# Performance work log

Measured on AMD Instinct MI355X. Metric: run time of the kernel, lower is better.

## Reference

```python
import jax, jax.numpy as jnp
import numpy as np

T, B, IN, H1, HB = 512, 256, 64, 128, 32  # seq, batch, input, LSTM width, bottleneck


def _lstm(x, w_ih, w_hh, b_ih, b_hh):
    """Single-layer unidirectional LSTM, time-major x: [T,B,in] -> [T,B,H].
    PyTorch gate order: i, f, g, o. Zero initial state."""
    H = w_hh.shape[1]
    # hoist input projection out of the scan: [T,B,4H]
    xg = jnp.einsum('tbi,gi->tbg', x, w_ih) + b_ih + b_hh

    def step(carry, xt):
        h, c = carry
        g = xt + h @ w_hh.T
        i, f, gg, o = jnp.split(g, 4, axis=-1)
        c = jax.nn.sigmoid(f) * c + jax.nn.sigmoid(i) * jnp.tanh(gg)
        h = jax.nn.sigmoid(o) * jnp.tanh(c)
        return (h, c), h

    h0 = jnp.zeros((x.shape[1], H), x.dtype)
    (_, _), hs = jax.lax.scan(step, (h0, h0), xg)
    return hs


def setup_inputs() -> dict:
    key = jax.random.key(0)
    ks = jax.random.split(key, 17)
    s = 0.05

    def p(k, shape):
        return jax.random.normal(k, shape, dtype=jnp.float32) * s

    return {
        'X': jax.random.normal(ks[0], (T, B, IN), dtype=jnp.float32),
        # en1: IN -> H1
        'w1_ih': p(ks[1], (4 * H1, IN)), 'w1_hh': p(ks[2], (4 * H1, H1)),
        'b1_ih': p(ks[3], (4 * H1,)), 'b1_hh': p(ks[4], (4 * H1,)),
        # en2: H1 -> HB
        'w2_ih': p(ks[5], (4 * HB, H1)), 'w2_hh': p(ks[6], (4 * HB, HB)),
        'b2_ih': p(ks[7], (4 * HB,)), 'b2_hh': p(ks[8], (4 * HB,)),
        # de1: HB -> H1
        'w3_ih': p(ks[9], (4 * H1, HB)), 'w3_hh': p(ks[10], (4 * H1, H1)),
        'b3_ih': p(ks[11], (4 * H1,)), 'b3_hh': p(ks[12], (4 * H1,)),
        # de2: H1 -> IN
        'w4_ih': p(ks[13], (4 * IN, H1)), 'w4_hh': p(ks[14], (4 * IN, IN)),
        'b4_ih': p(ks[15], (4 * IN,)), 'b4_hh': p(ks[16], (4 * IN,)),
    }


def reference(X, w1_ih, w1_hh, b1_ih, b1_hh, w2_ih, w2_hh, b2_ih, b2_hh,
              w3_ih, w3_hh, b3_ih, b3_hh, w4_ih, w4_hh, b4_ih, b4_hh):
    h = _lstm(X, w1_ih, w1_hh, b1_ih, b1_hh)      # [T,B,128]
    h = _lstm(h, w2_ih, w2_hh, b2_ih, b2_hh)      # [T,B,32]
    h = jnp.tanh(h)                               # bottleneck tanh
    h = _lstm(h, w3_ih, w3_hh, b3_ih, b3_hh)      # [T,B,128]
    out = _lstm(h, w4_ih, w4_hh, b4_ih, b4_hh)    # [T,B,64]
    return out
```

## Files before the change

kernel.cpp:

```cpp
#include <hip/hip_runtime.h>

#define T_STEPS 512
#define BATCH   256

typedef _Float16 f16;
typedef unsigned long long u64;
typedef __attribute__((ext_vector_type(8))) _Float16 f16x8;
typedef __attribute__((ext_vector_type(4))) _Float16 f16x4;
typedef __attribute__((ext_vector_type(4))) float    f32x4;

#define L2E 1.44269504088896340736f

__device__ __forceinline__ float rcp_f(float x)  { return __builtin_amdgcn_rcpf(x); }
__device__ __forceinline__ float exp2_f(float x) { return __builtin_amdgcn_exp2f(x); }

__device__ __forceinline__ float tanh_n(float x) {
    return fmaf(-2.0f, rcp_f(1.0f + exp2_f(2.0f * L2E * x)), 1.0f);
}
__device__ __forceinline__ u64 tanh4_f16(u64 v) {
    f16x4 h = __builtin_bit_cast(f16x4, v);
    f16x4 r;
#pragma unroll
    for (int i = 0; i < 4; ++i) r[i] = (f16)tanh_n((float)h[i]);
    return __builtin_bit_cast(u64, r);
}

__device__ __forceinline__ void barrier_lgkm() {
    asm volatile("s_waitcnt lgkmcnt(0)\n\ts_barrier" ::: "memory");
}
__device__ __forceinline__ void barrier_drain() {
    asm volatile("s_waitcnt vmcnt(0) lgkmcnt(0)\n\ts_barrier" ::: "memory");
}

__device__ __forceinline__ int  flag_load(const int* p) {
    return __hip_atomic_load(p, __ATOMIC_RELAXED, __HIP_MEMORY_SCOPE_AGENT);
}
__device__ __forceinline__ void flag_store(int* p, int v) {
    __hip_atomic_store(p, v, __ATOMIC_RELAXED, __HIP_MEMORY_SCOPE_AGENT);
}
__device__ __forceinline__ u64  panel_load(const u64* p) {
    return __hip_atomic_load(p, __ATOMIC_RELAXED, __HIP_MEMORY_SCOPE_AGENT);
}
__device__ __forceinline__ void panel_store(u64* p, u64 v) {
    __hip_atomic_store(p, v, __ATOMIC_RELAXED, __HIP_MEMORY_SCOPE_AGENT);
}

template <int IN_DIM, int H, bool IN_F32, bool OUT_PANEL, bool OUT_TANH>
__device__ __forceinline__ void lstm_layer_dev(
    char* sm,
    const void* __restrict__ xv,
    const int* in_flag,
    int* out_flag,
    const float* __restrict__ w_ih, const float* __restrict__ w_hh,
    const float* __restrict__ b_ih, const float* __restrict__ b_hh,
    void* __restrict__ outv,
    int group, int ltid)
{
    constexpr int KTX = IN_DIM / 32, KTH = H / 32, KT = KTX + KTH;
    constexpr int XP = IN_DIM + 8, HP = H + 8, NT = 4 * H;

    f16 (*xs)[16][XP] = (f16(*)[16][XP])sm;
    f16 (*hs)[16][HP] = (f16(*)[16][HP])(sm + 2 * 16 * XP * 2);

    const int wave = ltid >> 6, lane = ltid & 63;
    const int col = lane & 15, q = lane >> 4;
    const int bblk = group * 16;
    const int u = wave * 16 + col;

    f16x8 bw[4][KT];
#pragma unroll
    for (int g = 0; g < 4; ++g) {
        const float sc = (g == 2) ? 2.0f * L2E : L2E;
        const int row = g * H + u;
#pragma unroll
        for (int kt = 0; kt < KTX; ++kt) {
            const float* p = w_ih + (size_t)row * IN_DIM + kt * 32 + q * 8;
            f16x8 v;
#pragma unroll
            for (int j = 0; j < 8; ++j) v[j] = (f16)(p[j] * sc);
            bw[g][kt] = v;
        }
#pragma unroll
        for (int kt = 0; kt < KTH; ++kt) {
            const float* p = w_hh + (size_t)row * H + kt * 32 + q * 8;
            f16x8 v;
#pragma unroll
            for (int j = 0; j < 8; ++j) v[j] = (f16)(p[j] * sc);
            bw[g][KTX + kt] = v;
        }
    }
    float bias[4];
#pragma unroll
    for (int g = 0; g < 4; ++g)
        bias[g] = (b_ih[g * H + u] + b_hh[g * H + u]) * ((g == 2) ? 2.0f * L2E : L2E);
    float cst[4] = {0.f, 0.f, 0.f, 0.f};

    constexpr int ELD = IN_F32 ? 4 : 8;
    constexpr int EPR = IN_DIM / ELD;
    constexpr int NCH = 16 * EPR;
    constexpr int CPT = (NCH + NT - 1) / NT;
    constexpr long XADVB = (long)BATCH * IN_DIM * (IN_F32 ? 4 : 2);
    bool sv[CPT]; const char* sgp[CPT]; f16* slp[CPT];
    constexpr int LDSD = 16 * XP;
#pragma unroll
    for (int k = 0; k < CPT; ++k) {
        const int cc = ltid + k * NT;
        sv[k] = (cc < NCH);
        const int r_ = (cc < NCH ? cc : 0) / EPR;
        const int o_ = (cc < NCH ? cc : 0) % EPR;
        sgp[k] = (const char*)xv + ((size_t)(bblk + r_) * IN_DIM + o_ * ELD) * (IN_F32 ? 4 : 2);
        slp[k] = &xs[0][r_][o_ * ELD];
    }

    constexpr int OEPR = H / 4;
    u64* opg = nullptr;
    f16* olds = nullptr;
    float* outp_f32 = nullptr;
    if constexpr (OUT_PANEL) {
        const int orow = ltid / OEPR, ooff = ltid % OEPR;
        opg  = (u64*)((f16*)outv + (size_t)(bblk + orow) * H) + ooff;
        olds = &hs[0][orow][ooff * 4];
    } else {
        outp_f32 = (float*)outv + ((size_t)bblk + 4 * q) * H + u;
    }
    constexpr int HLDSD = 16 * HP;

    for (int i = ltid; i < 16 * HP; i += NT) hs[0][i / HP][i % HP] = (f16)0.f;
    int seen = 0;
    if constexpr (!IN_F32) {
        do { seen = flag_load(in_flag); } while (seen < 1);
    }
#pragma unroll
    for (int k = 0; k < CPT; ++k) {
        if (sv[k]) {
            if constexpr (IN_F32) {
                const f32x4 v = *reinterpret_cast<const f32x4*>(sgp[k]);
                f16x4 h4;
                h4[0] = (f16)v[0]; h4[1] = (f16)v[1]; h4[2] = (f16)v[2]; h4[3] = (f16)v[3];
                *reinterpret_cast<f16x4*>(slp[k]) = h4;
            } else {
                u64 a = panel_load((const u64*)sgp[k]);
                u64 b = panel_load((const u64*)sgp[k] + 1);
                u64 pk[2] = {a, b};
                *reinterpret_cast<f16x8*>(slp[k]) = *reinterpret_cast<const f16x8*>(pk);
            }
            sgp[k] += XADVB;
        }
    }
    barrier_drain();

    float hold[4] = {0.f, 0.f, 0.f, 0.f};

    auto step = [&](int t, int pbv, bool dodrain, bool dopub) {
        if constexpr (OUT_PANEL) {
            if (dopub && t >= 4 && ltid == 0) flag_store(out_flag, t - 1);
        }

        f32x4 xr32[CPT]; u64 xr16[CPT][2];
        const bool pf = (t + 1 < T_STEPS);
        if (pf) {
            if constexpr (!IN_F32) {
                if (seen < t + 2) {
                    do { seen = flag_load(in_flag); } while (seen < t + 2);
                }
            }
#pragma unroll
            for (int k = 0; k < CPT; ++k) {
                if (sv[k]) {
                    if constexpr (IN_F32) {
                        xr32[k] = *reinterpret_cast<const f32x4*>(sgp[k]);
                    } else {
                        xr16[k][0] = panel_load((const u64*)sgp[k]);
                        xr16[k][1] = panel_load((const u64*)sgp[k] + 1);
                    }
                    sgp[k] += XADVB;
                }
            }
        }

        if (t >= 1) {
            if constexpr (OUT_PANEL) {
                u64 v = *reinterpret_cast<const u64*>(olds + pbv * HLDSD);
                if constexpr (OUT_TANH) v = tanh4_f16(v);
                panel_store(opg, v);
                opg += (size_t)BATCH * H / 4;
            } else {
#pragma unroll
                for (int r = 0; r < 4; ++r) outp_f32[r * H] = hold[r];
                outp_f32 += (size_t)BATCH * H;
            }
        }

        f16x8 a[KT];
#pragma unroll
        for (int kt = 0; kt < KTX; ++kt)
            a[kt] = *reinterpret_cast<const f16x8*>(&xs[pbv][col][kt * 32 + q * 8]);
#pragma unroll
        for (int kt = 0; kt < KTH; ++kt)
            a[KTX + kt] = *reinterpret_cast<const f16x8*>(&hs[pbv][col][kt * 32 + q * 8]);

        f32x4 accX[4], accH[4];
#pragma unroll
        for (int g = 0; g < 4; ++g) {
            accX[g] = (f32x4){bias[g], bias[g], bias[g], bias[g]};
            accH[g] = (f32x4){0.f, 0.f, 0.f, 0.f};
        }
#pragma unroll
        for (int kt = 0; kt < KTX; ++kt)
#pragma unroll
            for (int g = 0; g < 4; ++g)
                accX[g] = __builtin_amdgcn_mfma_f32_16x16x32_f16(a[kt], bw[g][kt], accX[g], 0, 0, 0);
#pragma unroll
        for (int kt = 0; kt < KTH; ++kt)
#pragma unroll
            for (int g = 0; g < 4; ++g)
                accH[g] = __builtin_amdgcn_mfma_f32_16x16x32_f16(a[KTX + kt], bw[g][KTX + kt], accH[g], 0, 0, 0);

#pragma unroll
        for (int r = 0; r < 4; ++r) {
            const float yi = accX[0][r] + accH[0][r];
            const float yf = accX[1][r] + accH[1][r];
            const float yg = accX[2][r] + accH[2][r];
            const float yo = accX[3][r] + accH[3][r];
            const float Ei = exp2_f(-yi);
            const float G  = exp2_f(yg);
            const float Ef = exp2_f(-yf);
            const float sf = rcp_f(1.0f + Ef);
            const float itg = (2.0f * L2E) * (G - 1.0f) *
                              rcp_f((1.0f + Ei) * (G + 1.0f));
            cst[r] = fmaf(sf, cst[r], itg);
            const float C  = exp2_f(cst[r]);
            const float Eo = exp2_f(-yo);
            const float h  = (C - 1.0f) * rcp_f((1.0f + Eo) * (C + 1.0f));
            hs[pbv ^ 1][4 * q + r][u] = (f16)h;
            if constexpr (!OUT_PANEL) hold[r] = h;
        }

        if (pf) {
#pragma unroll
            for (int k = 0; k < CPT; ++k) {
                if (sv[k]) {
                    f16* dst = slp[k] + (pbv ^ 1) * LDSD;
                    if constexpr (IN_F32) {
                        f16x4 h4;
                        h4[0] = (f16)xr32[k][0]; h4[1] = (f16)xr32[k][1];
                        h4[2] = (f16)xr32[k][2]; h4[3] = (f16)xr32[k][3];
                        *reinterpret_cast<f16x4*>(dst) = h4;
                    } else {
                        *reinterpret_cast<f16x8*>(dst) =
                            *reinterpret_cast<const f16x8*>(xr16[k]);
                    }
                }
            }
        }

        if constexpr (!IN_F32) {
            if (dopub && seen < t + 9) seen = flag_load(in_flag);
        }

        if (dodrain) barrier_drain(); else barrier_lgkm();
    };

    for (int tb = 0; tb < T_STEPS; tb += 4) {
        step(tb + 0, 0, false, true);
        step(tb + 1, 1, false, false);
        step(tb + 2, 0, false, false);
        step(tb + 3, 1, true,  false);
    }

    if constexpr (OUT_PANEL) {
        u64 v = *reinterpret_cast<const u64*>(olds);
        if constexpr (OUT_TANH) v = tanh4_f16(v);
        panel_store(opg, v);
    } else {
#pragma unroll
        for (int r = 0; r < 4; ++r) outp_f32[r * H] = hold[r];
    }
    barrier_drain();
    if constexpr (OUT_PANEL) {
        if (ltid == 0) flag_store(out_flag, T_STEPS + 4);
    }
}

__global__ __launch_bounds__(512, 1)
void lstm_fused(const float* __restrict__ X,
                const float* __restrict__ w1_ih, const float* __restrict__ w1_hh,
                const float* __restrict__ b1_ih, const float* __restrict__ b1_hh,
                const float* __restrict__ w2_ih, const float* __restrict__ w2_hh,
                const float* __restrict__ b2_ih, const float* __restrict__ b2_hh,
                const float* __restrict__ w3_ih, const float* __restrict__ w3_hh,
                const float* __restrict__ b3_ih, const float* __restrict__ b3_hh,
                const float* __restrict__ w4_ih, const float* __restrict__ w4_hh,
                const float* __restrict__ b4_ih, const float* __restrict__ b4_hh,
                f16* __restrict__ h1, f16* __restrict__ h2, f16* __restrict__ h3,
                int* __restrict__ flags, float* __restrict__ out)
{
    __shared__ __attribute__((aligned(16))) char smem[45056];
    const int b = blockIdx.x, tid = threadIdx.x;

    if (b < 16) {
        lstm_layer_dev<64, 128, true, true, false>(
            smem, X, nullptr, flags + 0 * 16 + b,
            w1_ih, w1_hh, b1_ih, b1_hh, h1, b, tid);
    } else if (b < 20) {
        const int gl = tid >> 7;
        const int g  = (b - 16) * 4 + gl;
        lstm_layer_dev<128, 32, false, true, true>(
            smem + gl * 11264, h1, flags + 0 * 16 + g, flags + 1 * 16 + g,
            w2_ih, w2_hh, b2_ih, b2_hh, h2, g, tid & 127);
    } else if (b < 36) {
        const int g = b - 20;
        lstm_layer_dev<32, 128, false, true, false>(
            smem, h2, flags + 1 * 16 + g, flags + 2 * 16 + g,
            w3_ih, w3_hh, b3_ih, b3_hh, h3, g, tid);
    } else {
        const int gl = tid >> 8;
        const int g  = (b - 36) * 2 + gl;
        lstm_layer_dev<128, 64, false, false, false>(
            smem + gl * 13312, h3, flags + 2 * 16 + g, nullptr,
            w4_ih, w4_hh, b4_ih, b4_hh, out, g, tid & 255);
    }
}

extern "C" void kernel_launch(void* const* d_in, const int* in_sizes, int n_in,
                              void* d_out, int out_size, void* d_ws, size_t ws_size,
                              hipStream_t stream) {
    const float* X     = (const float*)d_in[0];
    const float* w1_ih = (const float*)d_in[1];
    const float* w1_hh = (const float*)d_in[2];
    const float* b1_ih = (const float*)d_in[3];
    const float* b1_hh = (const float*)d_in[4];
    const float* w2_ih = (const float*)d_in[5];
    const float* w2_hh = (const float*)d_in[6];
    const float* b2_ih = (const float*)d_in[7];
    const float* b2_hh = (const float*)d_in[8];
    const float* w3_ih = (const float*)d_in[9];
    const float* w3_hh = (const float*)d_in[10];
    const float* b3_ih = (const float*)d_in[11];
    const float* b3_hh = (const float*)d_in[12];
    const float* w4_ih = (const float*)d_in[13];
    const float* w4_hh = (const float*)d_in[14];
    const float* b4_ih = (const float*)d_in[15];
    const float* b4_hh = (const float*)d_in[16];

    float* out = (float*)d_out;

    int* flags = (int*)d_ws;
    f16* h1 = (f16*)((char*)d_ws + 256);
    f16* h2 = h1 + (size_t)T_STEPS * BATCH * 128;
    f16* h3 = h2 + (size_t)T_STEPS * BATCH * 32;

    lstm_fused<<<44, 512, 0, stream>>>(X,
        w1_ih, w1_hh, b1_ih, b1_hh, w2_ih, w2_hh, b2_ih, b2_hh,
        w3_ih, w3_hh, b3_ih, b3_hh, w4_ih, w4_hh, b4_ih, b4_hh,
        h1, h2, h3, flags, out);
}
```

Baseline: 667.0 us.

## Prefetch LSTM inputs two steps ahead and merge gate accumulators

The per-step global load of next-timestep inputs becomes a two-deep register pipeline: loads for step t+2 are issued during step t, using alternating odd/even register sets, and the drain barrier waits only until the newest loads remain outstanding. The separate input and hidden MFMA accumulators are merged into one chain seeded with the bias. This aims to hide global and inter-layer panel load latency behind the recurrent compute and to remove the final adds. In exchange it uses more registers, and the single accumulator chain lengthens the MFMA dependency chain.

```diff
diff --git a/kernel.cpp b/kernel.cpp
--- a/kernel.cpp
+++ b/kernel.cpp
@@ -30,6 +30,17 @@
 }
 __device__ __forceinline__ void barrier_drain() {
     asm volatile("s_waitcnt vmcnt(0) lgkmcnt(0)\n\ts_barrier" ::: "memory");
+}
+template <int K>
+__device__ __forceinline__ void barrier_drain_k() {
+    if constexpr (K == 1)
+        asm volatile("s_waitcnt vmcnt(1) lgkmcnt(0)\n\ts_barrier" ::: "memory");
+    else if constexpr (K == 2)
+        asm volatile("s_waitcnt vmcnt(2) lgkmcnt(0)\n\ts_barrier" ::: "memory");
+    else if constexpr (K == 4)
+        asm volatile("s_waitcnt vmcnt(4) lgkmcnt(0)\n\ts_barrier" ::: "memory");
+    else
+        asm volatile("s_waitcnt vmcnt(0) lgkmcnt(0)\n\ts_barrier" ::: "memory");
 }
 
 __device__ __forceinline__ int  flag_load(const int* p) {
@@ -99,6 +110,7 @@
     constexpr int EPR = IN_DIM / ELD;
     constexpr int NCH = 16 * EPR;
     constexpr int CPT = (NCH + NT - 1) / NT;
+    constexpr int NLOAD = IN_F32 ? CPT : 2 * CPT;
     constexpr long XADVB = (long)BATCH * IN_DIM * (IN_F32 ? 4 : 2);
     bool sv[CPT]; const char* sgp[CPT]; f16* slp[CPT];
     constexpr int LDSD = 16 * XP;
@@ -147,35 +159,32 @@
             sgp[k] += XADVB;
         }
     }
-    barrier_drain();
+    f32x4 xr32O[CPT], xr32E[CPT];
+    u64 xr16O[CPT][2], xr16E[CPT][2];
+    if constexpr (!IN_F32) {
+        if (seen < 2) { do { seen = flag_load(in_flag); } while (seen < 2); }
+    }
+#pragma unroll
+    for (int k = 0; k < CPT; ++k) {
+        if (sv[k]) {
+            if constexpr (IN_F32) {
+                xr32O[k] = *reinterpret_cast<const f32x4*>(sgp[k]);
+            } else {
+                xr16O[k][0] = panel_load((const u64*)sgp[k]);
+                xr16O[k][1] = panel_load((const u64*)sgp[k] + 1);
+            }
+            sgp[k] += XADVB;
+        }
+    }
+    barrier_lgkm();
 
     float hold[4] = {0.f, 0.f, 0.f, 0.f};
 
-    auto step = [&](int t, int pbv, bool dodrain, bool dopub) {
+    auto step = [&](int t, int pbv, bool dodrain, bool dopub,
+                    f32x4 (&c32)[CPT], f32x4 (&i32)[CPT],
+                    u64 (&c16)[CPT][2], u64 (&i16)[CPT][2]) {
         if constexpr (OUT_PANEL) {
             if (dopub && t >= 4 && ltid == 0) flag_store(out_flag, t - 1);
-        }
-
-        f32x4 xr32[CPT]; u64 xr16[CPT][2];
-        const bool pf = (t + 1 < T_STEPS);
-        if (pf) {
-            if constexpr (!IN_F32) {
-                if (seen < t + 2) {
-                    do { seen = flag_load(in_flag); } while (seen < t + 2);
-                }
-            }
-#pragma unroll
-            for (int k = 0; k < CPT; ++k) {
-                if (sv[k]) {
-                    if constexpr (IN_F32) {
-                        xr32[k] = *reinterpret_cast<const f32x4*>(sgp[k]);
-                    } else {
-                        xr16[k][0] = panel_load((const u64*)sgp[k]);
-                        xr16[k][1] = panel_load((const u64*)sgp[k] + 1);
-                    }
-                    sgp[k] += XADVB;
-                }
-            }
         }
 
         if (t >= 1) {
@@ -191,6 +200,27 @@
             }
         }
 
+        const bool iss = (t + 2 < T_STEPS);
+        if (iss) {
+            if constexpr (!IN_F32) {
+                if (seen < t + 3) {
+                    do { seen = flag_load(in_flag); } while (seen < t + 3);
+                }
+            }
+#pragma unroll
+            for (int k = 0; k < CPT; ++k) {
+                if (sv[k]) {
+                    if constexpr (IN_F32) {
+                        i32[k] = *reinterpret_cast<const f32x4*>(sgp[k]);
+                    } else {
+                        i16[k][0] = panel_load((const u64*)sgp[k]);
+                        i16[k][1] = panel_load((const u64*)sgp[k] + 1);
+                    }
+                    sgp[k] += XADVB;
+                }
+            }
+        }
+
         f16x8 a[KT];
 #pragma unroll
         for (int kt = 0; kt < KTX; ++kt)
@@ -199,29 +229,22 @@
         for (int kt = 0; kt < KTH; ++kt)
             a[KTX + kt] = *reinterpret_cast<const f16x8*>(&hs[pbv][col][kt * 32 + q * 8]);
 
-        f32x4 accX[4], accH[4];
-#pragma unroll
-        for (int g = 0; g < 4; ++g) {
-            accX[g] = (f32x4){bias[g], bias[g], bias[g], bias[g]};
-            accH[g] = (f32x4){0.f, 0.f, 0.f, 0.f};
-        }
-#pragma unroll
-        for (int kt = 0; kt < KTX; ++kt)
+        f32x4 acc[4];
+#pragma unroll
+        for (int g = 0; g < 4; ++g)
+            acc[g] = (f32x4){bias[g], bias[g], bias[g], bias[g]};
+#pragma unroll
+        for (int kt = 0; kt < KT; ++kt)
 #pragma unroll
             for (int g = 0; g < 4; ++g)
-                accX[g] = __builtin_amdgcn_mfma_f32_16x16x32_f16(a[kt], bw[g][kt], accX[g], 0, 0, 0);
-#pragma unroll
-        for (int kt = 0; kt < KTH; ++kt)
-#pragma unroll
-            for (int g = 0; g < 4; ++g)
-                accH[g] = __builtin_amdgcn_mfma_f32_16x16x32_f16(a[KTX + kt], bw[g][KTX + kt], accH[g], 0, 0, 0);
+                acc[g] = __builtin_amdgcn_mfma_f32_16x16x32_f16(a[kt], bw[g][kt], acc[g], 0, 0, 0);
 
 #pragma unroll
         for (int r = 0; r < 4; ++r) {
-            const float yi = accX[0][r] + accH[0][r];
-            const float yf = accX[1][r] + accH[1][r];
-            const float yg = accX[2][r] + accH[2][r];
-            const float yo = accX[3][r] + accH[3][r];
+            const float yi = acc[0][r];
+            const float yf = acc[1][r];
+            const float yg = acc[2][r];
+            const float yo = acc[3][r];
             const float Ei = exp2_f(-yi);
             const float G  = exp2_f(yg);
             const float Ef = exp2_f(-yf);
@@ -236,6 +259,7 @@
             if constexpr (!OUT_PANEL) hold[r] = h;
         }
 
+        const bool pf = (t + 1 < T_STEPS);
         if (pf) {
 #pragma unroll
             for (int k = 0; k < CPT; ++k) {
@@ -243,12 +267,12 @@
                     f16* dst = slp[k] + (pbv ^ 1) * LDSD;
                     if constexpr (IN_F32) {
                         f16x4 h4;
-                        h4[0] = (f16)xr32[k][0]; h4[1] = (f16)xr32[k][1];
-                        h4[2] = (f16)xr32[k][2]; h4[3] = (f16)xr32[k][3];
+                        h4[0] = (f16)c32[k][0]; h4[1] = (f16)c32[k][1];
+                        h4[2] = (f16)c32[k][2]; h4[3] = (f16)c32[k][3];
                         *reinterpret_cast<f16x4*>(dst) = h4;
                     } else {
                         *reinterpret_cast<f16x8*>(dst) =
-                            *reinterpret_cast<const f16x8*>(xr16[k]);
+                            *reinterpret_cast<const f16x8*>(c16[k]);
                     }
                 }
             }
@@ -258,14 +282,14 @@
             if (dopub && seen < t + 9) seen = flag_load(in_flag);
         }
 
-        if (dodrain) barrier_drain(); else barrier_lgkm();
+        if (dodrain) barrier_drain_k<NLOAD>(); else barrier_lgkm();
     };
 
     for (int tb = 0; tb < T_STEPS; tb += 4) {
-        step(tb + 0, 0, false, true);
-        step(tb + 1, 1, false, false);
-        step(tb + 2, 0, false, false);
-        step(tb + 3, 1, true,  false);
+        step(tb + 0, 0, false, true,  xr32O, xr32E, xr16O, xr16E);
+        step(tb + 1, 1, false, false, xr32E, xr32O, xr16E, xr16O);
+        step(tb + 2, 0, false, false, xr32O, xr32E, xr16O, xr16E);
+        step(tb + 3, 1, true,  false, xr32E, xr32O, xr16E, xr16O);
     }
 
     if constexpr (OUT_PANEL) {
```

Result: faster. 634.3 us (-4.9%).
